# Kernel tuning notes

Measured on AMD Instinct MI355X. Metric: run time of the kernel, lower is better.

Reference implementation:

```python
import jax, jax.numpy as jnp
import numpy as np

DECAY = 0.9
THRESH = 1.0
ALPHA = 25.0


def heaviside(x):
    # forward of the surrogate heaviside: hard step
    return (x > 0).astype(x.dtype)


def lif_layer(i_inj):
    """Run LIF recurrence over time. i_inj: [B, T, H] pre-computed input current."""
    B, T, H = i_inj.shape

    def step(carry, it):
        u, s = carry
        u_next = DECAY * (u - s * THRESH) + it
        s_next = heaviside(u_next - THRESH)
        return (u_next, s_next), s_next

    init = (jnp.zeros((B, H), i_inj.dtype), jnp.zeros((B, H), i_inj.dtype))
    _, spikes = jax.lax.scan(step, init, jnp.swapaxes(i_inj, 0, 1))  # [T, B, H]
    return jnp.swapaxes(spikes, 0, 1)  # [B, T, H]


def setup_inputs() -> dict:
    key = jax.random.key(0)
    ks = jax.random.split(key, 7)
    B, T, D, H, O = 32, 1024, 512, 512, 256
    x = jax.random.normal(ks[0], (B, T, D), dtype=jnp.float32)
    sD = 1.0 / np.sqrt(D)
    sH = 1.0 / np.sqrt(H)
    W0 = jax.random.uniform(ks[1], (H, D), jnp.float32, -sD, sD)
    b0 = jax.random.uniform(ks[2], (H,), jnp.float32, -sD, sD)
    W1 = jax.random.uniform(ks[3], (H, H), jnp.float32, -sH, sH)
    b1 = jax.random.uniform(ks[4], (H,), jnp.float32, -sH, sH)
    fc_W = jax.random.uniform(ks[5], (O, H), jnp.float32, -sH, sH)
    fc_b = jax.random.uniform(ks[6], (O,), jnp.float32, -sH, sH)
    return {"x": x, "W0": W0, "b0": b0, "W1": W1, "b1": b1, "fc_W": fc_W, "fc_b": fc_b}


def reference(x, W0, b0, W1, b1, fc_W, fc_b):
    # layer 0: batched input projection once, then time recurrence
    h = lif_layer(jnp.einsum('btd,hd->bth', x, W0) + b0)
    # layer 1 (dropout=0 -> identity)
    h = lif_layer(jnp.einsum('bth,gh->btg', h, W1) + b1)
    # last timestep, then fc head
    out = h[:, -1, :]
    return jnp.einsum('bh,oh->bo', out, fc_W) + fc_b
```

## Files before the change

kernel.cpp:

```cpp
#include <hip/hip_runtime.h>


#define DECAY 0.9f
#define THRESH 1.0f

constexpr int Bsz = 32;
constexpr int Tsz = 1024;
constexpr int Dsz = 512;
constexpr int Hsz = 512;
constexpr int Osz = 256;

using s16x8 = __attribute__((ext_vector_type(8))) short;
using f32x4 = __attribute__((ext_vector_type(4))) float;

__device__ __forceinline__ unsigned short f2bf_rne(float x) {
  unsigned b = __float_as_uint(x);
  return (unsigned short)((b + 0x7FFFu + ((b >> 16) & 1u)) >> 16);
}
__device__ __forceinline__ float bf2f(unsigned short h) {
  return __uint_as_float(((unsigned)h) << 16);
}

__global__ __launch_bounds__(256)
void wsplit2(const float* __restrict__ W0, unsigned short* __restrict__ h0,
             unsigned short* __restrict__ l0, const float* __restrict__ W1,
             unsigned short* __restrict__ h1, unsigned short* __restrict__ l1,
             int n) {
  const int i = blockIdx.x * 256 + threadIdx.x;
  if (i < n) {
    float w = W0[i];
    unsigned short h = f2bf_rne(w);
    h0[i] = h;
    l0[i] = f2bf_rne(w - bf2f(h));
    w = W1[i];
    h = f2bf_rne(w);
    h1[i] = h;
    l1[i] = f2bf_rne(w - bf2f(h));
  }
}

__global__ __launch_bounds__(256)
void xsplit(const float* __restrict__ x, unsigned short* __restrict__ xh,
            unsigned short* __restrict__ xl, int n4) {
  int i = blockIdx.x * 256 + threadIdx.x;
  const int stride = gridDim.x * 256;
  for (; i < n4; i += stride) {
    const float4 v = ((const float4*)x)[i];
    ushort4 hh, ll;
    hh.x = f2bf_rne(v.x); ll.x = f2bf_rne(v.x - bf2f(hh.x));
    hh.y = f2bf_rne(v.y); ll.y = f2bf_rne(v.y - bf2f(hh.y));
    hh.z = f2bf_rne(v.z); ll.z = f2bf_rne(v.z - bf2f(hh.z));
    hh.w = f2bf_rne(v.w); ll.w = f2bf_rne(v.w - bf2f(hh.w));
    ((ushort4*)xh)[i] = hh;
    ((ushort4*)xl)[i] = ll;
  }
}

typedef __attribute__((address_space(3))) unsigned int lds_u32;
typedef __attribute__((address_space(1))) unsigned int glb_u32;

__device__ __forceinline__ void gload_lds16(const void* g, void* l) {
  __builtin_amdgcn_global_load_lds(
      (glb_u32*)(unsigned long long)g,
      (lds_u32*)(unsigned int)(unsigned long long)l, 16, 0, 0);
}

template <int NAT>
__global__ __launch_bounds__(256)
void gemm_mfma(const unsigned short* __restrict__ A0,
               const unsigned short* __restrict__ A1,
               const unsigned short* __restrict__ Bhp,
               const unsigned short* __restrict__ Blp,
               const float* __restrict__ bias, float* __restrict__ C, int M) {
  constexpr int K = 512, N = 512;
  constexpr int NB = NAT + 2;
  __shared__ s16x8 sm[NB * 512];

  const int tid  = threadIdx.x;
  const int w    = tid >> 6;
  const int lane = tid & 63;
  const int wr   = w >> 1;
  const int wc   = w & 1;
  const int frow = lane & 15;
  const int kgrp = lane >> 4;
  const int swzf = (frow >> 1) & 3;
  const int cslot = kgrp ^ swzf;

  const int mtile = blockIdx.x * 128;
  const int ntile = blockIdx.y * 128;

  const unsigned short* srcs[NB];
  srcs[0] = A0;
  if (NAT == 2) srcs[1] = A1;
  srcs[NAT]     = Bhp;
  srcs[NAT + 1] = Blp;

  f32x4 acc[4][4];
#pragma unroll
  for (int i = 0; i < 4; ++i)
#pragma unroll
    for (int j = 0; j < 4; ++j) acc[i][j] = (f32x4){0.f, 0.f, 0.f, 0.f};

  for (int kt = 0; kt < K / 32; ++kt) {
    const int kbase = kt * 32;
    __syncthreads();
#pragma unroll
    for (int r = 0; r < 2; ++r) {
      const int chunk = r * 4 + w;
      const int li    = chunk * 64 + lane;
      const int row   = li >> 2;
      const int c     = li & 3;
      const int chg   = c ^ ((row >> 1) & 3);
      const int coff  = kbase + chg * 8;
#pragma unroll
      for (int buf = 0; buf < NB; ++buf) {
        const int rbase = (buf < NAT) ? mtile : ntile;
        gload_lds16(srcs[buf] + (size_t)(rbase + row) * K + coff,
                    &sm[buf * 512 + chunk * 64]);
      }
    }
    __syncthreads();

    s16x8 a0f[4], a1f[4], bhf[4], blf[4];
#pragma unroll
    for (int mi = 0; mi < 4; ++mi) {
      const int off = (wr * 64 + mi * 16 + frow) * 4 + cslot;
      a0f[mi] = sm[off];
      if (NAT == 2) a1f[mi] = sm[512 + off];
    }
#pragma unroll
    for (int nj = 0; nj < 4; ++nj) {
      const int off = (wc * 64 + nj * 16 + frow) * 4 + cslot;
      bhf[nj] = sm[NAT * 512 + off];
      blf[nj] = sm[(NAT + 1) * 512 + off];
    }
#pragma unroll
    for (int mi = 0; mi < 4; ++mi)
#pragma unroll
      for (int nj = 0; nj < 4; ++nj) {
        acc[mi][nj] = __builtin_amdgcn_mfma_f32_16x16x32_bf16(
            a0f[mi], bhf[nj], acc[mi][nj], 0, 0, 0);
        acc[mi][nj] = __builtin_amdgcn_mfma_f32_16x16x32_bf16(
            a0f[mi], blf[nj], acc[mi][nj], 0, 0, 0);
        if (NAT == 2) {
          acc[mi][nj] = __builtin_amdgcn_mfma_f32_16x16x32_bf16(
              a1f[mi], bhf[nj], acc[mi][nj], 0, 0, 0);
          acc[mi][nj] = __builtin_amdgcn_mfma_f32_16x16x32_bf16(
              a1f[mi], blf[nj], acc[mi][nj], 0, 0, 0);
        }
      }
  }

#pragma unroll
  for (int nj = 0; nj < 4; ++nj) {
    const int col = ntile + wc * 64 + nj * 16 + frow;
    const float b = bias[col];
#pragma unroll
    for (int mi = 0; mi < 4; ++mi) {
#pragma unroll
      for (int ri = 0; ri < 4; ++ri) {
        const int row = mtile + wr * 64 + mi * 16 + kgrp * 4 + ri;
        C[(size_t)row * N + col] = acc[mi][nj][ri] + b;
      }
    }
  }
}

__global__ __launch_bounds__(256)
void gemm_nt(const float* __restrict__ A, const float* __restrict__ W,
             const float* __restrict__ bias, float* __restrict__ C,
             int M, int N, int K) {
  __shared__ float4 As[128 * 4];
  __shared__ float4 Bs[128 * 4];

  const int tid  = threadIdx.x;
  const int w    = tid >> 6;
  const int lane = tid & 63;
  const int m0 = (w >> 1) * 64 + (lane >> 3) * 8;
  const int n0 = (w & 1)  * 64 + (lane & 7) * 8;

  const int mtile = blockIdx.x * 128;
  const int ntile = blockIdx.y * 128;

  const int sr  = tid >> 1;
  const int sc  = (tid & 1) * 2;
  const int swz = (sr >> 3) & 3;

  const float4* ag = (const float4*)(A + (size_t)(mtile + sr) * K);
  const float4* bg = (const float4*)(W + (size_t)(ntile + sr) * K);

  float acc[8][8];
#pragma unroll
  for (int i = 0; i < 8; ++i)
#pragma unroll
    for (int j = 0; j < 8; ++j) acc[i][j] = 0.f;

  for (int k0 = 0; k0 < K; k0 += 16) {
    const int kc4 = k0 >> 2;
    float4 av0 = ag[kc4 + sc], av1 = ag[kc4 + sc + 1];
    float4 bv0 = bg[kc4 + sc], bv1 = bg[kc4 + sc + 1];
    __syncthreads();
    As[sr * 4 + (sc ^ swz)] = av0;  As[sr * 4 + ((sc + 1) ^ swz)] = av1;
    Bs[sr * 4 + (sc ^ swz)] = bv0;  Bs[sr * 4 + ((sc + 1) ^ swz)] = bv1;
    __syncthreads();

#pragma unroll
    for (int kc = 0; kc < 4; ++kc) {
      float4 a4[8], b4[8];
#pragma unroll
      for (int i = 0; i < 8; ++i) {
        const int m = m0 + i;
        a4[i] = As[m * 4 + (kc ^ ((m >> 3) & 3))];
        const int n = n0 + i;
        b4[i] = Bs[n * 4 + (kc ^ ((n >> 3) & 3))];
      }
#pragma unroll
      for (int i = 0; i < 8; ++i)
#pragma unroll
        for (int j = 0; j < 8; ++j) {
          acc[i][j] += a4[i].x * b4[j].x;
          acc[i][j] += a4[i].y * b4[j].y;
          acc[i][j] += a4[i].z * b4[j].z;
          acc[i][j] += a4[i].w * b4[j].w;
        }
    }
  }

  float bb[8];
#pragma unroll
  for (int j = 0; j < 8; ++j) bb[j] = bias[ntile + n0 + j];
#pragma unroll
  for (int i = 0; i < 8; ++i) {
    float* cp = C + (size_t)(mtile + m0 + i) * N + ntile + n0;
    float4 o0, o1;
    o0.x = acc[i][0] + bb[0]; o0.y = acc[i][1] + bb[1];
    o0.z = acc[i][2] + bb[2]; o0.w = acc[i][3] + bb[3];
    o1.x = acc[i][4] + bb[4]; o1.y = acc[i][5] + bb[5];
    o1.z = acc[i][6] + bb[6]; o1.w = acc[i][7] + bb[7];
    ((float4*)cp)[0] = o0;
    ((float4*)cp)[1] = o1;
  }
}

constexpr int PF = 64;

__global__ __launch_bounds__(64)
void lif_spikes_bf16(const float* __restrict__ iin,
                     unsigned short* __restrict__ sout) {
  const int idx = blockIdx.x * 64 + threadIdx.x;
  const int b = idx >> 9, h = idx & 511;
  const float* p = iin + (size_t)b * Tsz * Hsz + h;
  unsigned short* q = sout + (size_t)b * Tsz * Hsz + h;

  float buf[PF];
#pragma unroll
  for (int j = 0; j < PF; ++j) buf[j] = p[(size_t)j * Hsz];

  float u = 0.f, s = 0.f;
  int t = 0;
  for (; t < Tsz - PF; t += PF) {
#pragma unroll
    for (int j = 0; j < PF; ++j) {
      const float cur = buf[j];
      buf[j] = p[(size_t)(t + PF + j) * Hsz];
      u = DECAY * (u - s * THRESH) + cur;
      s = (u > THRESH) ? 1.f : 0.f;
      q[(size_t)(t + j) * Hsz] =
          (u > THRESH) ? (unsigned short)0x3F80 : (unsigned short)0;
    }
  }
#pragma unroll
  for (int j = 0; j < PF; ++j) {
    const float cur = buf[j];
    u = DECAY * (u - s * THRESH) + cur;
    s = (u > THRESH) ? 1.f : 0.f;
    q[(size_t)(t + j) * Hsz] =
        (u > THRESH) ? (unsigned short)0x3F80 : (unsigned short)0;
  }
}

__global__ __launch_bounds__(64)
void lif_last_f32(const float* __restrict__ iin, float* __restrict__ sout) {
  const int idx = blockIdx.x * 64 + threadIdx.x;
  const int b = idx >> 9, h = idx & 511;
  const float* p = iin + (size_t)b * Tsz * Hsz + h;

  float buf[PF];
#pragma unroll
  for (int j = 0; j < PF; ++j) buf[j] = p[(size_t)j * Hsz];

  float u = 0.f, s = 0.f;
  int t = 0;
  for (; t < Tsz - PF; t += PF) {
#pragma unroll
    for (int j = 0; j < PF; ++j) {
      const float cur = buf[j];
      buf[j] = p[(size_t)(t + PF + j) * Hsz];
      u = DECAY * (u - s * THRESH) + cur;
      s = (u > THRESH) ? 1.f : 0.f;
    }
  }
#pragma unroll
  for (int j = 0; j < PF; ++j) {
    const float cur = buf[j];
    u = DECAY * (u - s * THRESH) + cur;
    s = (u > THRESH) ? 1.f : 0.f;
  }
  sout[idx] = s;
}

__global__ __launch_bounds__(256)
void fc_kernel(const float* __restrict__ sl, const float* __restrict__ fcW,
               const float* __restrict__ fcb, float* __restrict__ out) {
  const int b = blockIdx.x;
  const int o = threadIdx.x;
  const float4* wv = (const float4*)(fcW + (size_t)o * Hsz);
  const float4* sv = (const float4*)(sl + (size_t)b * Hsz);
  float acc = 0.f;
#pragma unroll 4
  for (int k = 0; k < Hsz / 4; ++k) {
    const float4 a = sv[k];
    const float4 ww = wv[k];
    acc += a.x * ww.x + a.y * ww.y + a.z * ww.z + a.w * ww.w;
  }
  out[(size_t)b * Osz + o] = acc + fcb[o];
}

extern "C" void kernel_launch(void* const* d_in, const int* in_sizes, int n_in,
                              void* d_out, int out_size, void* d_ws,
                              size_t ws_size, hipStream_t stream) {
  const float* x   = (const float*)d_in[0];
  const float* W0  = (const float*)d_in[1];
  const float* b0  = (const float*)d_in[2];
  const float* W1  = (const float*)d_in[3];
  const float* b1  = (const float*)d_in[4];
  const float* fcW = (const float*)d_in[5];
  const float* fcb = (const float*)d_in[6];
  float* out = (float*)d_out;

  constexpr size_t ELEMS = (size_t)Bsz * Tsz * Hsz;
  constexpr size_t WSZ   = (size_t)Hsz * Dsz;

  float*          ws   = (float*)d_ws;
  float*          i0   = ws;
  unsigned short* us0  = (unsigned short*)(ws + ELEMS);
  unsigned short* w1h  = us0 + ELEMS;
  unsigned short* w1l  = w1h + WSZ;
  float*          sl   = (float*)(w1l + WSZ);
  unsigned short* uxl  = (unsigned short*)(sl + (size_t)Bsz * Hsz);
  unsigned short* w0h  = uxl + ELEMS;
  unsigned short* w0l  = w0h + WSZ;
  float*          i1   = i0;

  const size_t need_full =
      (char*)(w0l + WSZ) - (char*)d_ws;
  const bool mfma1 = ws_size >= need_full;

  const int M = Bsz * Tsz;
  dim3 gtile(M / 128, Hsz / 128);

  if (mfma1) {
    wsplit2<<<(int)(WSZ / 256), 256, 0, stream>>>(W0, w0h, w0l, W1, w1h, w1l,
                                                  (int)WSZ);
    xsplit<<<2048, 256, 0, stream>>>(x, us0 , uxl, (int)(ELEMS / 4));
    gemm_mfma<2><<<gtile, 256, 0, stream>>>(us0, uxl, w0h, w0l, b0, i0, M);
  } else {
    wsplit2<<<(int)(WSZ / 256), 256, 0, stream>>>(W1, w1h, w1l, W1, w1h, w1l,
                                                  (int)WSZ);
    gemm_nt<<<gtile, 256, 0, stream>>>(x, W0, b0, i0, M, Hsz, Dsz);
  }

  lif_spikes_bf16<<<(Bsz * Hsz) / 64, 64, 0, stream>>>(i0, us0);

  gemm_mfma<1><<<gtile, 256, 0, stream>>>(us0, nullptr, w1h, w1l, b1, i1, M);

  lif_last_f32<<<(Bsz * Hsz) / 64, 64, 0, stream>>>(i1, sl);

  fc_kernel<<<Bsz, Osz, 0, stream>>>(sl, fcW, fcb, out);
}
```

Before: 287.2 us.

## Use producer-consumer warps with LDS double buffering in LIF scan kernels

Replaces the per-thread register-prefetch LIF kernels with a 256-thread block in which three producer wavefronts stream 64-timestep chunks of input current into double-buffered LDS via gload_lds16. One consumer wavefront runs the serial recurrence from LDS. The goal is to hide global-memory latency of the strided time loads behind the dependent scan. The cost is a block-wide barrier per chunk, and only a quarter of the threads do the compute.

After: 273.5 us. 1.05x faster.

```diff
diff --git a/kernel.cpp b/kernel.cpp
--- a/kernel.cpp
+++ b/kernel.cpp
@@ -242,71 +242,61 @@
   }
 }
 
-constexpr int PF = 64;
-
-__global__ __launch_bounds__(64)
-void lif_spikes_bf16(const float* __restrict__ iin,
-                     unsigned short* __restrict__ sout) {
-  const int idx = blockIdx.x * 64 + threadIdx.x;
-  const int b = idx >> 9, h = idx & 511;
-  const float* p = iin + (size_t)b * Tsz * Hsz + h;
-  unsigned short* q = sout + (size_t)b * Tsz * Hsz + h;
-
-  float buf[PF];
-#pragma unroll
-  for (int j = 0; j < PF; ++j) buf[j] = p[(size_t)j * Hsz];
+template <bool STORE>
+__global__ __launch_bounds__(256)
+void lif_pc(const float* __restrict__ iin, unsigned short* __restrict__ sout,
+            float* __restrict__ lastout) {
+  constexpr int C = 64;
+  constexpr int NC = Tsz / C;
+  __shared__ float lds[2][C][64];
+
+  const int tid  = threadIdx.x;
+  const int w    = tid >> 6;
+  const int lane = tid & 63;
+  const int b    = blockIdx.x >> 3;
+  const int h0   = (blockIdx.x & 7) * 64;
+
+  const float* base = iin + (size_t)b * Tsz * Hsz + h0;
+
+  const int rb  = (w == 1) ? 0 : (w == 2) ? 24 : 44;
+  const int cnt = (w == 1) ? 6 : 5;
+
+#define LIF_STAGE(kk, nb)                                                    \
+  if (w != 0) {                                                              \
+    for (int j = 0; j < cnt; ++j) {                                          \
+      const int row = rb + j * 4;                                            \
+      const float* g =                                                       \
+          base + (size_t)((kk)*C + row + (lane >> 4)) * Hsz + (lane & 15) * 4;\
+      gload_lds16(g, &lds[nb][row][0]);                                      \
+    }                                                                        \
+  }
+
+  LIF_STAGE(0, 0);
+  __syncthreads();
 
   float u = 0.f, s = 0.f;
-  int t = 0;
-  for (; t < Tsz - PF; t += PF) {
-#pragma unroll
-    for (int j = 0; j < PF; ++j) {
-      const float cur = buf[j];
-      buf[j] = p[(size_t)(t + PF + j) * Hsz];
-      u = DECAY * (u - s * THRESH) + cur;
-      s = (u > THRESH) ? 1.f : 0.f;
-      q[(size_t)(t + j) * Hsz] =
-          (u > THRESH) ? (unsigned short)0x3F80 : (unsigned short)0;
-    }
-  }
-#pragma unroll
-  for (int j = 0; j < PF; ++j) {
-    const float cur = buf[j];
-    u = DECAY * (u - s * THRESH) + cur;
-    s = (u > THRESH) ? 1.f : 0.f;
-    q[(size_t)(t + j) * Hsz] =
-        (u > THRESH) ? (unsigned short)0x3F80 : (unsigned short)0;
-  }
-}
-
-__global__ __launch_bounds__(64)
-void lif_last_f32(const float* __restrict__ iin, float* __restrict__ sout) {
-  const int idx = blockIdx.x * 64 + threadIdx.x;
-  const int b = idx >> 9, h = idx & 511;
-  const float* p = iin + (size_t)b * Tsz * Hsz + h;
-
-  float buf[PF];
-#pragma unroll
-  for (int j = 0; j < PF; ++j) buf[j] = p[(size_t)j * Hsz];
-
-  float u = 0.f, s = 0.f;
-  int t = 0;
-  for (; t < Tsz - PF; t += PF) {
-#pragma unroll
-    for (int j = 0; j < PF; ++j) {
-      const float cur = buf[j];
-      buf[j] = p[(size_t)(t + PF + j) * Hsz];
-      u = DECAY * (u - s * THRESH) + cur;
-      s = (u > THRESH) ? 1.f : 0.f;
-    }
-  }
-#pragma unroll
-  for (int j = 0; j < PF; ++j) {
-    const float cur = buf[j];
-    u = DECAY * (u - s * THRESH) + cur;
-    s = (u > THRESH) ? 1.f : 0.f;
-  }
-  sout[idx] = s;
+  unsigned short* q =
+      STORE ? sout + (size_t)b * Tsz * Hsz + h0 + lane : (unsigned short*)0;
+
+  for (int k = 0; k < NC; ++k) {
+    if (k + 1 < NC) LIF_STAGE(k + 1, (k + 1) & 1);
+    if (w == 0) {
+      const int cb = k & 1;
+#pragma unroll 16
+      for (int t = 0; t < C; ++t) {
+        const float cur = lds[cb][t][lane];
+        u = DECAY * (u - s * THRESH) + cur;
+        s = (u > THRESH) ? 1.f : 0.f;
+        if (STORE)
+          q[(size_t)(k * C + t) * Hsz] =
+              (u > THRESH) ? (unsigned short)0x3F80 : (unsigned short)0;
+      }
+    }
+    __syncthreads();
+  }
+#undef LIF_STAGE
+
+  if (!STORE && w == 0) lastout[(size_t)b * Hsz + h0 + lane] = s;
 }
 
 __global__ __launch_bounds__(256)
@@ -370,11 +360,11 @@
     gemm_nt<<<gtile, 256, 0, stream>>>(x, W0, b0, i0, M, Hsz, Dsz);
   }
 
-  lif_spikes_bf16<<<(Bsz * Hsz) / 64, 64, 0, stream>>>(i0, us0);
+  lif_pc<true><<<Bsz * 8, 256, 0, stream>>>(i0, us0, nullptr);
 
   gemm_mfma<1><<<gtile, 256, 0, stream>>>(us0, nullptr, w1h, w1l, b1, i1, M);
 
-  lif_last_f32<<<(Bsz * Hsz) / 64, 64, 0, stream>>>(i1, sl);
+  lif_pc<false><<<Bsz * 8, 256, 0, stream>>>(i1, nullptr, sl);
 
   fc_kernel<<<Bsz, Osz, 0, stream>>>(sl, fcW, fcb, out);
 }
```
